# Performance work log

Hardware: AMD Instinct MI355X
Metric: run time of the kernel (lower is better)

Reference implementation:

```python
import jax, jax.numpy as jnp
import numpy as np

EPS = 1e-7  # K.epsilon()
NUM_ROUTING = 3

def squash(s, axis=-1):
    sq = jnp.sum(jnp.square(s), axis=axis, keepdims=True)
    scale = sq / (1.0 + sq) / jnp.sqrt(sq + EPS)
    return scale * s

def setup_inputs() -> dict:
    key = jax.random.key(0)
    k1, k2 = jax.random.split(key)
    B, INC, IND = 512, 1152, 8   # batch, input_num_capsule, input_dim_capsule
    NC, DC = 10, 16              # num_capsule, dim_capsule
    inputs = jax.random.normal(k1, (B, INC, IND), dtype=jnp.float32)
    W = jax.random.normal(k2, (NC, INC, DC, IND), dtype=jnp.float32) * 0.05
    return {"inputs": inputs, "W": W}

def reference(inputs, W):
    # u_hat[b,j,i,d] = sum_k inputs[b,i,k] * W[j,i,d,k]
    u_hat = jnp.einsum('bik,jidk->bjid', inputs, W)  # [B, NC, INC, DC]
    b = jnp.zeros(u_hat.shape[:3], dtype=u_hat.dtype)  # [B, NC, INC]
    v = None
    for i in range(NUM_ROUTING):
        c = jax.nn.softmax(b, axis=1)                  # softmax over output capsules
        s = jnp.einsum('bji,bjid->bjd', c, u_hat)      # weighted sum over input caps
        v = squash(s)                                  # [B, NC, DC]
        if i < NUM_ROUTING - 1:
            b = b + jnp.einsum('bjd,bjid->bji', v, u_hat)  # agreement update
    return v
```

## Files before the change

### kernel.cpp

```cpp
#include <hip/hip_runtime.h>


#define NB 512
#define NI 1152
#define NJ 10
#define ND 16

typedef short          bf16x8 __attribute__((ext_vector_type(8)));
typedef unsigned short u16x8  __attribute__((ext_vector_type(8)));
typedef float          f32x4  __attribute__((ext_vector_type(4)));

constexpr float EPS_ = 1e-7f;

constexpr size_t XB_ELEMS = (size_t)NB * NI * 8;
constexpr size_t WB_ELEMS = (size_t)NJ * NI * ND * 8;
constexpr int    XQ = 1179648;
constexpr int    WQ = 368640;
constexpr int    NIGB = 144;

__device__ inline unsigned short f2bf(float f) {
    unsigned u = __float_as_uint(f);
    return (unsigned short)((u + 0x7fffu + ((u >> 16) & 1u)) >> 16);
}
__device__ inline float bf2f(unsigned short u) {
    return __uint_as_float((unsigned)u << 16);
}

__global__ __launch_bounds__(256)
void conv_bf16(const float* __restrict__ x, const float* __restrict__ Wg,
               unsigned short* __restrict__ xb, unsigned short* __restrict__ wb)
{
    int t = blockIdx.x * 256 + threadIdx.x;
    if (t < XQ) {
        float4 v = ((const float4*)x)[t];
        ushort4 o; o.x=f2bf(v.x); o.y=f2bf(v.y); o.z=f2bf(v.z); o.w=f2bf(v.w);
        ((ushort4*)xb)[t] = o;
    } else if (t - XQ < WQ) {
        int u = t - XQ;
        float4 v = ((const float4*)Wg)[u];
        ushort4 o; o.x=f2bf(v.x); o.y=f2bf(v.y); o.z=f2bf(v.z); o.w=f2bf(v.w);
        ((ushort4*)wb)[u] = o;
    }
}

template <int MODE>
__global__ __launch_bounds__(256, 2)
void caps_pass(const unsigned short* __restrict__ xb,
               const unsigned short* __restrict__ wb,
               const float* __restrict__ vsum_g,
               unsigned short* __restrict__ part)
{
    __shared__ __align__(16) char smem[30368];
    unsigned short* wl = (unsigned short*)smem;
    unsigned short* xl = (unsigned short*)(smem + 20608);

    const int tid = threadIdx.x, lane = tid & 63, w = tid >> 6;
    const int bl = lane & 15, kg = lane >> 4;
    const int bg = blockIdx.x, ig = blockIdx.y;
    const int i0 = ig * 8, b0 = bg * 64;
    const int b  = b0 + w * 16 + bl;
    const int brow = w * 16 + bl;

#pragma unroll
    for (int r = 0; r < 5; ++r) {
        int g  = tid + r * 256;
        int il = g / 160, rem = g - il * 160;
        const unsigned short* src =
            wb + ((size_t)(rem >> 4) * NI + (i0 + il)) * 128 + (rem & 15) * 8;
        *(u16x8*)(wl + (il * 161 + rem) * 8) = *(const u16x8*)src;
    }
#pragma unroll
    for (int r = 0; r < 2; ++r) {
        int g = tid + r * 256;
        if (g < 512) {
            int br = g >> 3, il = g & 7;
            *(u16x8*)(xl + (br * 9 + il) * 8) =
                *(const u16x8*)(xb + ((size_t)(b0 + br) * NI + i0 + il) * 8);
        }
    }

    f32x4 vs[NJ];
    if (MODE == 1) {
#pragma unroll
        for (int j = 0; j < NJ; ++j)
            vs[j] = *(const f32x4*)(vsum_g + (size_t)b * 160 + j * 16 + kg * 4);
    }

    __syncthreads();

    const f32x4  zero  = {0.f, 0.f, 0.f, 0.f};
    const bf16x8 zerob = {0, 0, 0, 0, 0, 0, 0, 0};
    f32x4 sacc[NJ];
#pragma unroll
    for (int j = 0; j < NJ; ++j) sacc[j] = zero;

#pragma unroll
    for (int t4 = 0; t4 < 2; ++t4) {
        bf16x8 afull[NJ];
#pragma unroll
        for (int j = 0; j < NJ; ++j)
            afull[j] = *(const bf16x8*)(wl + (((t4 * 4 + kg) * 161) + j * 16 + bl) * 8);

        if (MODE == 0) {
            bf16x8 xv = *(const bf16x8*)(xl + (brow * 9 + t4 * 4 + kg) * 8);
#pragma unroll
            for (int j = 0; j < NJ; ++j)
                sacc[j] = __builtin_amdgcn_mfma_f32_16x16x32_bf16(afull[j], xv, sacc[j], 0, 0, 0);
        } else {
            bf16x8 xv = *(const bf16x8*)(xl + (brow * 9 + t4 * 4 + kg) * 8);
#pragma unroll
            for (int q = 0; q < 4; ++q) {
                const bf16x8 bq = (kg == q) ? xv : zerob;
                f32x4 uh[NJ];
#pragma unroll
                for (int j = 0; j < NJ; ++j)
                    uh[j] = __builtin_amdgcn_mfma_f32_16x16x32_bf16(afull[j], bq, zero, 0, 0, 0);

                float bd[NJ];
#pragma unroll
                for (int j = 0; j < NJ; ++j) {
                    float v = uh[j][0] * vs[j][0] + uh[j][1] * vs[j][1]
                            + uh[j][2] * vs[j][2] + uh[j][3] * vs[j][3];
                    v += __shfl_xor(v, 16, 64);
                    v += __shfl_xor(v, 32, 64);
                    bd[j] = v;
                }
                float m01 = fmaxf(bd[0], bd[1]), m23 = fmaxf(bd[2], bd[3]);
                float m45 = fmaxf(bd[4], bd[5]), m67 = fmaxf(bd[6], bd[7]);
                float m89 = fmaxf(bd[8], bd[9]);
                float m = fmaxf(fmaxf(fmaxf(m01, m23), fmaxf(m45, m67)), m89);
#pragma unroll
                for (int j = 0; j < NJ; ++j) bd[j] = __expf(bd[j] - m);
                float Z = ((bd[0] + bd[1]) + (bd[2] + bd[3]))
                        + ((bd[4] + bd[5]) + (bd[6] + bd[7])) + (bd[8] + bd[9]);
                const float rZ = 1.f / Z;
#pragma unroll
                for (int j = 0; j < NJ; ++j) {
                    const float c = bd[j] * rZ;
                    sacc[j] += c * uh[j];
                }
            }
        }
    }

    __syncthreads();
    unsigned short* s16 = (unsigned short*)smem;
#pragma unroll
    for (int j = 0; j < NJ; ++j) {
        ushort4 o;
        o.x = f2bf(sacc[j][0]); o.y = f2bf(sacc[j][1]);
        o.z = f2bf(sacc[j][2]); o.w = f2bf(sacc[j][3]);
        *(ushort4*)(s16 + brow * 168 + j * 16 + kg * 4) = o;
    }
    __syncthreads();
    unsigned short* pp = part + ((size_t)ig * NB + b0) * 160;
#pragma unroll
    for (int r = 0; r < 5; ++r) {
        int idx = tid + r * 256;
        int row = idx / 20, ch = idx - row * 20;
        *(u16x8*)(pp + idx * 8) = *(const u16x8*)(s16 + row * 168 + ch * 8);
    }
}

__global__ __launch_bounds__(256)
void squash_reduce(const unsigned short* __restrict__ part,
                   float* __restrict__ vsum_g, float* __restrict__ out,
                   float alpha, int mode)
{
    const int t = blockIdx.x * 256 + threadIdx.x;
    const unsigned short* p = part + t;
    float a0 = 0.f, a1 = 0.f, a2 = 0.f, a3 = 0.f;
#pragma unroll 4
    for (int ig = 0; ig < NIGB; ig += 4) {
        a0 += bf2f(p[(size_t)ig * 81920]);
        a1 += bf2f(p[(size_t)(ig + 1) * 81920]);
        a2 += bf2f(p[(size_t)(ig + 2) * 81920]);
        a3 += bf2f(p[(size_t)(ig + 3) * 81920]);
    }
    const float s = ((a0 + a1) + (a2 + a3)) * alpha;

    float sq = s * s;
    sq += __shfl_xor(sq, 1, 64);
    sq += __shfl_xor(sq, 2, 64);
    sq += __shfl_xor(sq, 4, 64);
    sq += __shfl_xor(sq, 8, 64);
    const float sc = sq / ((1.f + sq) * sqrtf(sq + EPS_));
    const float v  = sc * s;

    if (mode == 0)      vsum_g[t] = v;
    else if (mode == 1) vsum_g[t] += v;
    else                out[t] = v;
}

extern "C" void kernel_launch(void* const* d_in, const int* in_sizes, int n_in,
                              void* d_out, int out_size, void* d_ws, size_t ws_size,
                              hipStream_t stream)
{
    const float* inp = (const float*)d_in[0];
    const float* Wg  = (const float*)d_in[1];
    float* out = (float*)d_out;

    unsigned short* xbp  = (unsigned short*)d_ws;
    unsigned short* wbp  = xbp + XB_ELEMS;
    unsigned short* part = wbp + WB_ELEMS;
    float* vsum = (float*)(part + (size_t)NIGB * NB * 160);

    conv_bf16<<<(XQ + WQ + 255) / 256, 256, 0, stream>>>(inp, Wg, xbp, wbp);

    dim3 grid(8, NIGB);
    caps_pass<0><<<grid, 256, 0, stream>>>(xbp, wbp, nullptr, part);
    squash_reduce<<<320, 256, 0, stream>>>(part, vsum, out, 0.1f, 0);
    caps_pass<1><<<grid, 256, 0, stream>>>(xbp, wbp, vsum, part);
    squash_reduce<<<320, 256, 0, stream>>>(part, vsum, out, 1.0f, 1);
    caps_pass<1><<<grid, 256, 0, stream>>>(xbp, wbp, vsum, part);
    squash_reduce<<<320, 256, 0, stream>>>(part, vsum, out, 1.0f, 2);
}
```

Measured before the change: 163.8 us.

## Fuse routing iterations into one cooperative kernel with grid syncs

Replaces the six alternating caps_pass/squash_reduce launches with one cooperative kernel of 512 blocks. Each block loads 18 input capsules of W and x into LDS once and keeps them resident across all three routing iterations, using grid.sync between the partial-sum and squash phases. This removes repeated launches and repeated global reloads, and it cuts partials from 144 to 64 groups. The costs are roughly 66KB of shared memory per block, which can limit residency at two blocks per CU, plus grid-wide barrier overhead, padding-wasted MFMAs in the last tile, and a fallback path if the cooperative launch fails.

```diff
diff --git a/kernel.cpp b/kernel.cpp
--- a/kernel.cpp
+++ b/kernel.cpp
@@ -1,4 +1,7 @@
 #include <hip/hip_runtime.h>
+#include <hip/hip_cooperative_groups.h>
+
+namespace cg = cooperative_groups;
 
 
 #define NB 512
@@ -16,6 +19,7 @@
 constexpr size_t WB_ELEMS = (size_t)NJ * NI * ND * 8;
 constexpr int    XQ = 1179648;
 constexpr int    WQ = 368640;
+constexpr int    NIGC = 64;
 constexpr int    NIGB = 144;
 
 __device__ inline unsigned short f2bf(float f) {
@@ -43,12 +47,171 @@
     }
 }
 
+
+__global__ __launch_bounds__(256, 2)
+void caps_fused(const unsigned short* __restrict__ xb,
+                const unsigned short* __restrict__ wb,
+                unsigned short* __restrict__ part,
+                float* __restrict__ vsum_g,
+                float* __restrict__ out)
+{
+    __shared__ __align__(16) char smem[65840];
+    unsigned short* wl = (unsigned short*)smem;
+    unsigned short* xl = (unsigned short*)(smem + 46368);
+    unsigned short* zp = (unsigned short*)(smem + 65824);
+
+    const int tid = threadIdx.x, lane = tid & 63, w = tid >> 6;
+    const int bl = lane & 15, kg = lane >> 4;
+    const int blk = blockIdx.x;
+    const int bg = blk & 7, igc = blk >> 3;
+    const int i0 = igc * 18, b0 = bg * 64;
+    const int brow = w * 16 + bl;
+    const int b  = b0 + brow;
+    const int gt = blk * 256 + tid;
+
+    if (tid < 8) zp[tid] = 0;
+
+#pragma unroll
+    for (int r = 0; r < 12; ++r) {
+        int g = tid + r * 256;
+        if (g < 2880) {
+            int il = g / 160, rem = g - il * 160;
+            *(u16x8*)(wl + (il * 161 + rem) * 8) = *(const u16x8*)(
+                wb + ((size_t)(rem >> 4) * NI + (i0 + il)) * 128 + (rem & 15) * 8);
+        }
+    }
+#pragma unroll
+    for (int r = 0; r < 5; ++r) {
+        int g = tid + r * 256;
+        if (g < 1152) {
+            int br = g / 18, il = g - br * 18;
+            *(u16x8*)(xl + (br * 19 + il) * 8) = *(const u16x8*)(
+                xb + ((size_t)(b0 + br) * NI + i0 + il) * 8);
+        }
+    }
+    __syncthreads();
+
+    cg::grid_group grid = cg::this_grid();
+
+    const f32x4  zero  = {0.f, 0.f, 0.f, 0.f};
+    const bf16x8 zerob = {0, 0, 0, 0, 0, 0, 0, 0};
+    float vr = 0.f;
+
+    for (int iter = 0; iter < 3; ++iter) {
+        const bool fused = (iter > 0);
+
+        f32x4 vs[NJ];
+        if (fused) {
+#pragma unroll
+            for (int j = 0; j < NJ; ++j)
+                vs[j] = *(const f32x4*)(vsum_g + (size_t)b * 160 + j * 16 + kg * 4);
+        }
+
+        f32x4 sacc[NJ];
+#pragma unroll
+        for (int j = 0; j < NJ; ++j) sacc[j] = zero;
+
+#pragma unroll
+        for (int t4 = 0; t4 < 5; ++t4) {
+            const int nq = (t4 == 4) ? 2 : 4;
+            const int il = t4 * 4 + kg;
+            const bool realA = (il < 18);
+
+            bf16x8 afull[NJ];
+#pragma unroll
+            for (int j = 0; j < NJ; ++j) {
+                const unsigned short* ap = realA
+                    ? (wl + (il * 161 + j * 16 + bl) * 8) : zp;
+                afull[j] = *(const bf16x8*)ap;
+            }
+            const int xil = (t4 == 4) ? (16 + (kg & 1)) : il;
+            bf16x8 xv = *(const bf16x8*)(xl + (brow * 19 + xil) * 8);
+
+            if (!fused) {
+#pragma unroll
+                for (int j = 0; j < NJ; ++j)
+                    sacc[j] = __builtin_amdgcn_mfma_f32_16x16x32_bf16(afull[j], xv, sacc[j], 0, 0, 0);
+            } else {
+#pragma unroll
+                for (int q = 0; q < 4; ++q) {
+                    if (q < nq) {
+                        const bf16x8 bq = (kg == q) ? xv : zerob;
+                        f32x4 uh[NJ];
+#pragma unroll
+                        for (int j = 0; j < NJ; ++j)
+                            uh[j] = __builtin_amdgcn_mfma_f32_16x16x32_bf16(afull[j], bq, zero, 0, 0, 0);
+
+                        float bd[NJ];
+#pragma unroll
+                        for (int j = 0; j < NJ; ++j) {
+                            float v = uh[j][0] * vs[j][0] + uh[j][1] * vs[j][1]
+                                    + uh[j][2] * vs[j][2] + uh[j][3] * vs[j][3];
+                            v += __shfl_xor(v, 16, 64);
+                            v += __shfl_xor(v, 32, 64);
+                            bd[j] = v;
+                        }
+                        float m01 = fmaxf(bd[0], bd[1]), m23 = fmaxf(bd[2], bd[3]);
+                        float m45 = fmaxf(bd[4], bd[5]), m67 = fmaxf(bd[6], bd[7]);
+                        float m89 = fmaxf(bd[8], bd[9]);
+                        float m = fmaxf(fmaxf(fmaxf(m01, m23), fmaxf(m45, m67)), m89);
+#pragma unroll
+                        for (int j = 0; j < NJ; ++j) bd[j] = __expf(bd[j] - m);
+                        float Z = ((bd[0] + bd[1]) + (bd[2] + bd[3]))
+                                + ((bd[4] + bd[5]) + (bd[6] + bd[7])) + (bd[8] + bd[9]);
+                        const float rZ = 1.f / Z;
+#pragma unroll
+                        for (int j = 0; j < NJ; ++j) {
+                            const float c = bd[j] * rZ;
+                            sacc[j] += c * uh[j];
+                        }
+                    }
+                }
+            }
+        }
+
+        unsigned short* pp = part + (size_t)igc * 81920 + (size_t)b * 160 + kg * 4;
+#pragma unroll
+        for (int j = 0; j < NJ; ++j) {
+            ushort4 o;
+            o.x = f2bf(sacc[j][0]); o.y = f2bf(sacc[j][1]);
+            o.z = f2bf(sacc[j][2]); o.w = f2bf(sacc[j][3]);
+            *(ushort4*)(pp + j * 16) = o;
+        }
+
+        grid.sync();
+
+        if (gt < 81920) {
+            const unsigned short* p = part + gt;
+            float a0 = 0.f, a1 = 0.f, a2 = 0.f, a3 = 0.f;
+#pragma unroll 4
+            for (int c = 0; c < NIGC; c += 4) {
+                a0 += bf2f(p[(size_t)c * 81920]);
+                a1 += bf2f(p[(size_t)(c + 1) * 81920]);
+                a2 += bf2f(p[(size_t)(c + 2) * 81920]);
+                a3 += bf2f(p[(size_t)(c + 3) * 81920]);
+            }
+            float s = ((a0 + a1) + (a2 + a3)) * (iter == 0 ? 0.1f : 1.0f);
+            float sq = s * s;
+            sq += __shfl_xor(sq, 1, 64);
+            sq += __shfl_xor(sq, 2, 64);
+            sq += __shfl_xor(sq, 4, 64);
+            sq += __shfl_xor(sq, 8, 64);
+            const float sc = sq / ((1.f + sq) * sqrtf(sq + EPS_));
+            const float v  = sc * s;
+            if (iter < 2) { vr += v; vsum_g[gt] = vr; }
+            else          out[gt] = v;
+        }
+        if (iter < 2) grid.sync();
+    }
+}
+
+
 template <int MODE>
 __global__ __launch_bounds__(256, 2)
-void caps_pass(const unsigned short* __restrict__ xb,
-               const unsigned short* __restrict__ wb,
-               const float* __restrict__ vsum_g,
-               unsigned short* __restrict__ part)
+void caps_fb(const unsigned short* __restrict__ xb,
+             const unsigned short* __restrict__ wb,
+             const float* __restrict__ vsum_g,
+             unsigned short* __restrict__ part)
 {
     __shared__ __align__(16) char smem[30368];
     unsigned short* wl = (unsigned short*)smem;
@@ -65,9 +228,8 @@
     for (int r = 0; r < 5; ++r) {
         int g  = tid + r * 256;
         int il = g / 160, rem = g - il * 160;
-        const unsigned short* src =
-            wb + ((size_t)(rem >> 4) * NI + (i0 + il)) * 128 + (rem & 15) * 8;
-        *(u16x8*)(wl + (il * 161 + rem) * 8) = *(const u16x8*)src;
+        *(u16x8*)(wl + (il * 161 + rem) * 8) = *(const u16x8*)(
+            wb + ((size_t)(rem >> 4) * NI + (i0 + il)) * 128 + (rem & 15) * 8);
     }
 #pragma unroll
     for (int r = 0; r < 2; ++r) {
@@ -85,7 +247,6 @@
         for (int j = 0; j < NJ; ++j)
             vs[j] = *(const f32x4*)(vsum_g + (size_t)b * 160 + j * 16 + kg * 4);
     }
-
     __syncthreads();
 
     const f32x4  zero  = {0.f, 0.f, 0.f, 0.f};
@@ -100,14 +261,13 @@
 #pragma unroll
         for (int j = 0; j < NJ; ++j)
             afull[j] = *(const bf16x8*)(wl + (((t4 * 4 + kg) * 161) + j * 16 + bl) * 8);
+        bf16x8 xv = *(const bf16x8*)(xl + (brow * 9 + t4 * 4 + kg) * 8);
 
         if (MODE == 0) {
-            bf16x8 xv = *(const bf16x8*)(xl + (brow * 9 + t4 * 4 + kg) * 8);
 #pragma unroll
             for (int j = 0; j < NJ; ++j)
                 sacc[j] = __builtin_amdgcn_mfma_f32_16x16x32_bf16(afull[j], xv, sacc[j], 0, 0, 0);
         } else {
-            bf16x8 xv = *(const bf16x8*)(xl + (brow * 9 + t4 * 4 + kg) * 8);
 #pragma unroll
             for (int q = 0; q < 4; ++q) {
                 const bf16x8 bq = (kg == q) ? xv : zerob;
@@ -115,7 +275,6 @@
 #pragma unroll
                 for (int j = 0; j < NJ; ++j)
                     uh[j] = __builtin_amdgcn_mfma_f32_16x16x32_bf16(afull[j], bq, zero, 0, 0, 0);
-
                 float bd[NJ];
 #pragma unroll
                 for (int j = 0; j < NJ; ++j) {
@@ -125,10 +284,9 @@
                     v += __shfl_xor(v, 32, 64);
                     bd[j] = v;
                 }
-                float m01 = fmaxf(bd[0], bd[1]), m23 = fmaxf(bd[2], bd[3]);
-                float m45 = fmaxf(bd[4], bd[5]), m67 = fmaxf(bd[6], bd[7]);
-                float m89 = fmaxf(bd[8], bd[9]);
-                float m = fmaxf(fmaxf(fmaxf(m01, m23), fmaxf(m45, m67)), m89);
+                float m = fmaxf(fmaxf(fmaxf(fmaxf(bd[0], bd[1]), fmaxf(bd[2], bd[3])),
+                                      fmaxf(fmaxf(bd[4], bd[5]), fmaxf(bd[6], bd[7]))),
+                                fmaxf(bd[8], bd[9]));
 #pragma unroll
                 for (int j = 0; j < NJ; ++j) bd[j] = __expf(bd[j] - m);
                 float Z = ((bd[0] + bd[1]) + (bd[2] + bd[3]))
@@ -163,9 +321,9 @@
 }
 
 __global__ __launch_bounds__(256)
-void squash_reduce(const unsigned short* __restrict__ part,
-                   float* __restrict__ vsum_g, float* __restrict__ out,
-                   float alpha, int mode)
+void squash_fb(const unsigned short* __restrict__ part,
+               float* __restrict__ vsum_g, float* __restrict__ out,
+               float alpha, int mode)
 {
     const int t = blockIdx.x * 256 + threadIdx.x;
     const unsigned short* p = part + t;
@@ -178,7 +336,6 @@
         a3 += bf2f(p[(size_t)(ig + 3) * 81920]);
     }
     const float s = ((a0 + a1) + (a2 + a3)) * alpha;
-
     float sq = s * s;
     sq += __shfl_xor(sq, 1, 64);
     sq += __shfl_xor(sq, 2, 64);
@@ -186,11 +343,11 @@
     sq += __shfl_xor(sq, 8, 64);
     const float sc = sq / ((1.f + sq) * sqrtf(sq + EPS_));
     const float v  = sc * s;
-
     if (mode == 0)      vsum_g[t] = v;
     else if (mode == 1) vsum_g[t] += v;
     else                out[t] = v;
 }
+
 
 extern "C" void kernel_launch(void* const* d_in, const int* in_sizes, int n_in,
                               void* d_out, int out_size, void* d_ws, size_t ws_size,
@@ -207,11 +364,16 @@
 
     conv_bf16<<<(XQ + WQ + 255) / 256, 256, 0, stream>>>(inp, Wg, xbp, wbp);
 
-    dim3 grid(8, NIGB);
-    caps_pass<0><<<grid, 256, 0, stream>>>(xbp, wbp, nullptr, part);
-    squash_reduce<<<320, 256, 0, stream>>>(part, vsum, out, 0.1f, 0);
-    caps_pass<1><<<grid, 256, 0, stream>>>(xbp, wbp, vsum, part);
-    squash_reduce<<<320, 256, 0, stream>>>(part, vsum, out, 1.0f, 1);
-    caps_pass<1><<<grid, 256, 0, stream>>>(xbp, wbp, vsum, part);
-    squash_reduce<<<320, 256, 0, stream>>>(part, vsum, out, 1.0f, 2);
-}
+    void* args[] = {(void*)&xbp, (void*)&wbp, (void*)&part, (void*)&vsum, (void*)&out};
+    hipError_t rc = hipLaunchCooperativeKernel((const void*)caps_fused,
+                                               dim3(512), dim3(256), args, 0, stream);
+    if (rc != hipSuccess) {
+        dim3 grid(8, NIGB);
+        caps_fb<0><<<grid, 256, 0, stream>>>(xbp, wbp, nullptr, part);
+        squash_fb<<<320, 256, 0, stream>>>(part, vsum, out, 0.1f, 0);
+        caps_fb<1><<<grid, 256, 0, stream>>>(xbp, wbp, vsum, part);
+        squash_fb<<<320, 256, 0, stream>>>(part, vsum, out, 1.0f, 1);
+        caps_fb<1><<<grid, 256, 0, stream>>>(xbp, wbp, vsum, part);
+        squash_fb<<<320, 256, 0, stream>>>(part, vsum, out, 1.0f, 2);
+    }
+}
```

Result: slower. 449.9 us (+174.7%).
